# Kernel optimization log

Hardware: AMD Instinct MI355X
Metric: run time of the kernel (lower is better)

The kernel has to match this reference:

```python
import jax, jax.numpy as jnp
import numpy as np

B, S, D, H = 4, 2048, 1024, 16
HD = D // H  # head_dim = 64


def setup_inputs() -> dict:
    key = jax.random.key(0)
    kx, kq, kk, kv, ko = jax.random.split(key, 5)
    scale = 1.0 / np.sqrt(D)
    return {
        "x": jax.random.normal(kx, (B, S, D), dtype=jnp.float32),
        "wq": jax.random.normal(kq, (D, D), dtype=jnp.float32) * scale,
        "wk": jax.random.normal(kk, (D, D), dtype=jnp.float32) * scale,
        "wv": jax.random.normal(kv, (D, D), dtype=jnp.float32) * scale,
        "wo": jax.random.normal(ko, (D, D), dtype=jnp.float32) * scale,
    }


def reference(x, wq, wk, wv, wo):
    b, s, d = x.shape
    # nn.Linear stores weight [out, in]: y = x @ W.T
    q = (x @ wq.T).reshape(b, s, H, HD)
    k = (x @ wk.T).reshape(b, s, H, HD)
    v = (x @ wv.T).reshape(b, s, H, HD)
    # scores: [b, h, s, s]
    scores = jnp.einsum("bqhd,bkhd->bhqk", q, k) / np.sqrt(HD)
    causal = jnp.triu(jnp.ones((s, s), dtype=bool), k=1)
    scores = jnp.where(causal, -jnp.inf, scores)
    attn = jax.nn.softmax(scores, axis=-1)
    out = jnp.einsum("bhqk,bkhd->bqhd", attn, v).reshape(b, s, d)
    return out @ wo.T
```

## Files before the change

### kernel.cpp

```cpp
#include <hip/hip_runtime.h>
#include <math.h>

typedef unsigned short u16;
typedef __attribute__((ext_vector_type(8))) short short8;
typedef __attribute__((ext_vector_type(4))) short short4v;
typedef __attribute__((ext_vector_type(4))) float f32x4;
typedef __attribute__((ext_vector_type(2))) unsigned int uint2v;

constexpr int Bn = 4, Sn = 2048, Dn = 1024, Hn = 16;
constexpr float SCL = 0.125f * 1.44269504f;

__device__ __forceinline__ u16 f2bf(float f) {
  unsigned u = __float_as_uint(f);
  u += 0x7fffu + ((u >> 16) & 1u);
  return (u16)(u >> 16);
}

__device__ __forceinline__ f32x4 mfma32(short8 a, short8 b, f32x4 c) {
  return __builtin_amdgcn_mfma_f32_16x16x32_bf16(a, b, c, 0, 0, 0);
}

__device__ __forceinline__ f32x4 mfma16(short4v a, short4v b, f32x4 c) {
#if __has_builtin(__builtin_amdgcn_mfma_f32_16x16x16_bf16)
  return __builtin_amdgcn_mfma_f32_16x16x16_bf16(a, b, c, 0, 0, 0);
#elif __has_builtin(__builtin_amdgcn_mfma_f32_16x16x16bf16_1k)
  return __builtin_amdgcn_mfma_f32_16x16x16bf16_1k(a, b, c, 0, 0, 0);
#else
  short8 a8 = {a[0], a[1], a[2], a[3], 0, 0, 0, 0};
  short8 b8 = {b[0], b[1], b[2], b[3], 0, 0, 0, 0};
  return __builtin_amdgcn_mfma_f32_16x16x32_bf16(a8, b8, c, 0, 0, 0);
#endif
}

__device__ __forceinline__ void gl_lds16(const u16* g, u16* l) {
  __builtin_amdgcn_global_load_lds(
      (const __attribute__((address_space(1))) unsigned int*)g,
      (__attribute__((address_space(3))) unsigned int*)l, 16, 0, 0);
}

__global__ __launch_bounds__(256) void cast_all(
    const float4* __restrict__ x, const float4* __restrict__ wq,
    const float4* __restrict__ wk, const float4* __restrict__ wv,
    const float4* __restrict__ wo, ushort4* __restrict__ xb,
    ushort4* __restrict__ wqb, ushort4* __restrict__ wkb,
    ushort4* __restrict__ wvb, ushort4* __restrict__ wob) {
  const int blk = blockIdx.x;
  const float4* in;
  ushort4* out;
  int base;
  float s = 1.0f;
  if (blk < 8192) {
    in = x; out = xb; base = blk;
  } else if (blk < 9216) {
    in = wq; out = wqb; base = blk - 8192; s = SCL;
  } else if (blk < 10240) {
    in = wk; out = wkb; base = blk - 9216;
  } else if (blk < 11264) {
    in = wv; out = wvb; base = blk - 10240;
  } else {
    in = wo; out = wob; base = blk - 11264;
  }
  const int i = base * 256 + threadIdx.x;
  const float4 f = in[i];
  ushort4 o;
  o.x = f2bf(f.x * s); o.y = f2bf(f.y * s);
  o.z = f2bf(f.z * s); o.w = f2bf(f.w * s);
  out[i] = o;
}

template <int MODE>
__device__ __forceinline__ void gemm_body(const u16* __restrict__ A,
                                          const u16* __restrict__ W,
                                          u16* __restrict__ Cb,
                                          float* __restrict__ Cf,
                                          int bx, int by) {
  __shared__ u16 Asm[128 * 32];
  __shared__ u16 Wsm[128 * 32];
  const int t = threadIdx.x;
  const int w = t >> 6, l = t & 63;
  const int wy = w >> 1, wx = w & 1;
  const int q = l >> 4, r = l & 15;
  const int m0 = bx * 128, n0 = by * 128;
  const int c0 = w * 64 + l;

  f32x4 acc[4][4] = {};

  for (int k0 = 0; k0 < 1024; k0 += 32) {
    __syncthreads();
#pragma unroll
    for (int i = 0; i < 2; ++i) {
      const int c = c0 + i * 256;
      const int row = c >> 2, cl = c & 3;
      const int cg = cl ^ ((row >> 1) & 3);
      gl_lds16(A + (size_t)(m0 + row) * 1024 + k0 + cg * 8, &Asm[c * 8]);
      gl_lds16(W + (size_t)(n0 + row) * 1024 + k0 + cg * 8, &Wsm[c * 8]);
    }
    __syncthreads();

    short8 af[4], bf[4];
#pragma unroll
    for (int mi = 0; mi < 4; ++mi) {
      const int rowA = wy * 64 + mi * 16 + r;
      af[mi] = *(const short8*)&Asm[rowA * 32 + (q ^ ((rowA >> 1) & 3)) * 8];
      const int rowB = wx * 64 + mi * 16 + r;
      bf[mi] = *(const short8*)&Wsm[rowB * 32 + (q ^ ((rowB >> 1) & 3)) * 8];
    }
#pragma unroll
    for (int mi = 0; mi < 4; ++mi)
#pragma unroll
      for (int ni = 0; ni < 4; ++ni)
        acc[mi][ni] = mfma32(af[mi], bf[ni], acc[mi][ni]);
  }

  if (MODE == 2) {
    const int bq = m0 >> 11;
    const int jt = ((m0 & 2047) >> 6) + wy;
    const int hh = (n0 >> 6) + wx;
    u16* vt_t = Cb + ((size_t)((bq * 16 + hh) * 32) + jt) * 4096;
#pragma unroll
    for (int mi = 0; mi < 4; ++mi)
#pragma unroll
      for (int ni = 0; ni < 4; ++ni) {
        short4v pk;
#pragma unroll
        for (int e = 0; e < 4; ++e) pk[e] = (short)f2bf(acc[mi][ni][e]);
        const int hd = ni * 16 + r;
        const int c2 = q + 4 * (mi >> 1);
        *(short4v*)&vt_t[hd * 64 + ((c2 ^ (r & 7)) * 8) + (mi & 1) * 4] = pk;
      }
    return;
  }

#pragma unroll
  for (int mi = 0; mi < 4; ++mi) {
    const int row = m0 + wy * 64 + mi * 16 + q * 4;
#pragma unroll
    for (int ni = 0; ni < 4; ++ni) {
      const int col = n0 + wx * 64 + ni * 16 + r;
#pragma unroll
      for (int e = 0; e < 4; ++e) {
        if (MODE == 1)
          Cf[(size_t)(row + e) * 1024 + col] = acc[mi][ni][e];
        else
          Cb[(size_t)(row + e) * 1024 + col] = f2bf(acc[mi][ni][e]);
      }
    }
  }
}

__global__ __launch_bounds__(256) void gemm_qkv(const u16* __restrict__ A,
                                                const u16* __restrict__ Wq,
                                                const u16* __restrict__ Wk,
                                                const u16* __restrict__ Wv,
                                                u16* __restrict__ Cq,
                                                u16* __restrict__ Ck,
                                                u16* __restrict__ Vt) {
  const int z = blockIdx.z;
  if (z == 2)
    gemm_body<2>(A, Wv, Vt, nullptr, blockIdx.x, blockIdx.y);
  else
    gemm_body<0>(A, z ? Wk : Wq, z ? Ck : Cq, nullptr, blockIdx.x, blockIdx.y);
}

__global__ __launch_bounds__(256) void gemm_out(const u16* __restrict__ A,
                                                const u16* __restrict__ W,
                                                float* __restrict__ C) {
  gemm_body<1>(A, W, nullptr, C, blockIdx.x, blockIdx.y);
}

__global__ __launch_bounds__(128) void attn_v6(const u16* __restrict__ Qb,
                                               const u16* __restrict__ Kb,
                                               const u16* __restrict__ Vt,
                                               u16* __restrict__ Ob) {
  const int i = blockIdx.x;
  const int grp = (i & 7) + 8 * (i >> 7);
  const int qp = (i >> 3) & 15;
  const int b = grp >> 4, h = grp & 15;
  const int t = threadIdx.x;
  const int w = t >> 6, l = t & 63;
  const int q = l >> 4, r = l & 15;

  __shared__ u16 Kd[2][4096];
  __shared__ u16 Vd[2][4096];

  const size_t kgbase = (size_t)(b * Sn) * Dn + h * 64;
  const size_t vgbase = (size_t)((b * Hn + h) * 32) * 4096;

  const u16* kg[4];
  const u16* vg[4];
#pragma unroll
  for (int ii = 0; ii < 4; ++ii) {
    const int c = t + ii * 128, row = c >> 3, cl = c & 7;
    kg[ii] = Kb + kgbase + (size_t)row * Dn + (cl ^ (row & 7)) * 8;
    vg[ii] = Vt + vgbase + c * 8;
  }
  const int rx = r & 7;
  const int b0 = r * 64 + ((q ^ rx) * 8);
  const int b1 = r * 64 + (((4 + q) ^ rx) * 8);

#pragma unroll 1
  for (int ph = 0; ph < 2; ++ph) {
    const int st = ph ? 31 - qp : qp;
    const int qb64 = st * 64;

    short8 Qf[2][2];
#pragma unroll
    for (int mi = 0; mi < 2; ++mi)
#pragma unroll
      for (int kf = 0; kf < 2; ++kf)
        Qf[mi][kf] = *(const short8*)(Qb +
            (size_t)(b * Sn + qb64 + w * 32 + mi * 16 + r) * Dn + h * 64 +
            kf * 32 + q * 8);

    f32x4 O[2][4] = {};
    float l_[2] = {0.f, 0.f};

    __syncthreads();
#pragma unroll
    for (int ii = 0; ii < 4; ++ii) {
      const int c8 = (t + ii * 128) * 8;
      gl_lds16(kg[ii], &Kd[0][c8]);
      gl_lds16(vg[ii], &Vd[0][c8]);
    }
    const u16* kgt[4];
    const u16* vgt[4];
#pragma unroll
    for (int ii = 0; ii < 4; ++ii) {
      kgt[ii] = kg[ii] + 64 * Dn;
      vgt[ii] = vg[ii] + 4096;
    }

    for (int jt = 0; jt <= st; ++jt) {
      __syncthreads();
      if (jt < st) {
        u16* kl = &Kd[(jt + 1) & 1][0];
        u16* vl = &Vd[(jt + 1) & 1][0];
#pragma unroll
        for (int ii = 0; ii < 4; ++ii) {
          const int c8 = (t + ii * 128) * 8;
          gl_lds16(kgt[ii], kl + c8);
          gl_lds16(vgt[ii], vl + c8);
          kgt[ii] += 64 * Dn;
          vgt[ii] += 4096;
        }
      }
      const u16* KtA = &Kd[jt & 1][b0];
      const u16* KtB = &Kd[jt & 1][b1];

      short8 Kf[4][2];
#pragma unroll
      for (int ni = 0; ni < 4; ++ni) {
        Kf[ni][0] = *(const short8*)(KtA + ni * 1024);
        Kf[ni][1] = *(const short8*)(KtB + ni * 1024);
      }

      f32x4 S[2][4] = {};
      __builtin_amdgcn_s_setprio(1);
#pragma unroll
      for (int ni = 0; ni < 4; ++ni)
#pragma unroll
        for (int kf = 0; kf < 2; ++kf) {
          S[0][ni] = mfma32(Kf[ni][kf], Qf[0][kf], S[0][ni]);
          S[1][ni] = mfma32(Kf[ni][kf], Qf[1][kf], S[1][ni]);
        }
      __builtin_amdgcn_s_setprio(0);

      if (jt == st) {
#pragma unroll
        for (int mi = 0; mi < 2; ++mi) {
          const int qrow = w * 32 + mi * 16 + r;
#pragma unroll
          for (int ni = 0; ni < 4; ++ni) {
            const int key = ni * 16 + q * 4;
#pragma unroll
            for (int e = 0; e < 4; ++e)
              if (key + e > qrow) S[mi][ni][e] = -3.0e38f;
          }
        }
      }

      short4v Pf[2][4];
#pragma unroll
      for (int mi = 0; mi < 2; ++mi)
#pragma unroll
        for (int ni = 0; ni < 4; ++ni) {
          const float p0 = __builtin_amdgcn_exp2f(S[mi][ni][0]);
          const float p1 = __builtin_amdgcn_exp2f(S[mi][ni][1]);
          const float p2 = __builtin_amdgcn_exp2f(S[mi][ni][2]);
          const float p3 = __builtin_amdgcn_exp2f(S[mi][ni][3]);
          l_[mi] += (p0 + p1) + (p2 + p3);
          unsigned plo, phi;
          asm("v_cvt_pk_bf16_f32 %0, %1, %2" : "=v"(plo) : "v"(p0), "v"(p1));
          asm("v_cvt_pk_bf16_f32 %0, %1, %2" : "=v"(phi) : "v"(p2), "v"(p3));
          const uint2v pk2 = {plo, phi};
          Pf[mi][ni] = __builtin_bit_cast(short4v, pk2);
        }

      const u16* VsA = &Vd[jt & 1][b0];
      const u16* VsB = &Vd[jt & 1][b1];
      __builtin_amdgcn_s_setprio(1);
#pragma unroll
      for (int np = 0; np < 2; ++np)
#pragma unroll
        for (int ni2 = 0; ni2 < 4; ++ni2) {
          const short8 vv =
              *(const short8*)((np ? VsB : VsA) + ni2 * 1024);
          const short4v va = {vv[0], vv[1], vv[2], vv[3]};
          const short4v vb2 = {vv[4], vv[5], vv[6], vv[7]};
          O[0][ni2] = mfma16(va, Pf[0][2 * np], O[0][ni2]);
          O[0][ni2] = mfma16(vb2, Pf[0][2 * np + 1], O[0][ni2]);
          O[1][ni2] = mfma16(va, Pf[1][2 * np], O[1][ni2]);
          O[1][ni2] = mfma16(vb2, Pf[1][2 * np + 1], O[1][ni2]);
        }
      __builtin_amdgcn_s_setprio(0);
    }

#pragma unroll
    for (int mi = 0; mi < 2; ++mi) {
      float s = l_[mi];
      s += __shfl_xor(s, 16, 64);
      s += __shfl_xor(s, 32, 64);
      const float rl = __builtin_amdgcn_rcpf(s);
#pragma unroll
      for (int ni2 = 0; ni2 < 4; ++ni2) {
        short4v o;
#pragma unroll
        for (int e = 0; e < 4; ++e) o[e] = (short)f2bf(O[mi][ni2][e] * rl);
        *(short4v*)(Ob + (size_t)(b * Sn + qb64 + w * 32 + mi * 16 + r) * Dn +
                    h * 64 + ni2 * 16 + q * 4) = o;
      }
    }
  }
}

extern "C" void kernel_launch(void* const* d_in, const int* in_sizes, int n_in,
                              void* d_out, int out_size, void* d_ws, size_t ws_size,
                              hipStream_t stream) {
  const float* x  = (const float*)d_in[0];
  const float* wq = (const float*)d_in[1];
  const float* wk = (const float*)d_in[2];
  const float* wv = (const float*)d_in[3];
  const float* wo = (const float*)d_in[4];
  float* out = (float*)d_out;

  u16* xb  = (u16*)d_ws;
  u16* wqb = xb + 8388608;
  u16* wkb = wqb + 1048576;
  u16* wvb = wkb + 1048576;
  u16* wob = wvb + 1048576;
  u16* qb  = wob + 1048576;
  u16* kb  = qb + 8388608;
  u16* vt2 = kb + 8388608;
  u16* aob = vt2 + 8388608;

  cast_all<<<12288, 256, 0, stream>>>(
      (const float4*)x, (const float4*)wq, (const float4*)wk,
      (const float4*)wv, (const float4*)wo, (ushort4*)xb, (ushort4*)wqb,
      (ushort4*)wkb, (ushort4*)wvb, (ushort4*)wob);

  gemm_qkv<<<dim3(64, 8, 3), 256, 0, stream>>>(xb, wqb, wkb, wvb, qb, kb, vt2);

  attn_v6<<<1024, 128, 0, stream>>>(qb, kb, vt2, aob);

  gemm_out<<<dim3(64, 8), 256, 0, stream>>>(aob, wob, out);
}
```

Baseline: 240.8 us.

## Load attention K/V straight into registers, split query tiles into more blocks, widen GEMM K-step

The attention kernel drops LDS staging and barriers. Each wave now loads K and V fragments directly from global memory into registers, with K prefetched one tile ahead through a ping-pong register pair. Each block handles one query tile instead of two paired tiles, so the grid doubles, and an interleaved mapping keeps the load balanced. The V-transpose store drops its XOR swizzle to match the new direct-read pattern, and the QKV/out GEMMs move to a 64-wide K step with an 8-way swizzle, halving barrier count. Risks include redundant global K/V traffic across the two waves and higher register pressure.

```diff
diff --git a/kernel.cpp b/kernel.cpp
--- a/kernel.cpp
+++ b/kernel.cpp
@@ -74,42 +74,43 @@
                                           u16* __restrict__ Cb,
                                           float* __restrict__ Cf,
                                           int bx, int by) {
-  __shared__ u16 Asm[128 * 32];
-  __shared__ u16 Wsm[128 * 32];
+  __shared__ u16 Asm[128 * 64];
+  __shared__ u16 Wsm[128 * 64];
   const int t = threadIdx.x;
   const int w = t >> 6, l = t & 63;
   const int wy = w >> 1, wx = w & 1;
   const int q = l >> 4, r = l & 15;
   const int m0 = bx * 128, n0 = by * 128;
-  const int c0 = w * 64 + l;
 
   f32x4 acc[4][4] = {};
 
-  for (int k0 = 0; k0 < 1024; k0 += 32) {
+  for (int k0 = 0; k0 < 1024; k0 += 64) {
     __syncthreads();
 #pragma unroll
-    for (int i = 0; i < 2; ++i) {
-      const int c = c0 + i * 256;
-      const int row = c >> 2, cl = c & 3;
-      const int cg = cl ^ ((row >> 1) & 3);
+    for (int i = 0; i < 4; ++i) {
+      const int c = t + i * 256;
+      const int row = c >> 3, cl = c & 7;
+      const int cg = cl ^ (row & 7);
       gl_lds16(A + (size_t)(m0 + row) * 1024 + k0 + cg * 8, &Asm[c * 8]);
       gl_lds16(W + (size_t)(n0 + row) * 1024 + k0 + cg * 8, &Wsm[c * 8]);
     }
     __syncthreads();
-
-    short8 af[4], bf[4];
-#pragma unroll
-    for (int mi = 0; mi < 4; ++mi) {
-      const int rowA = wy * 64 + mi * 16 + r;
-      af[mi] = *(const short8*)&Asm[rowA * 32 + (q ^ ((rowA >> 1) & 3)) * 8];
-      const int rowB = wx * 64 + mi * 16 + r;
-      bf[mi] = *(const short8*)&Wsm[rowB * 32 + (q ^ ((rowB >> 1) & 3)) * 8];
-    }
-#pragma unroll
-    for (int mi = 0; mi < 4; ++mi)
-#pragma unroll
-      for (int ni = 0; ni < 4; ++ni)
-        acc[mi][ni] = mfma32(af[mi], bf[ni], acc[mi][ni]);
+#pragma unroll
+    for (int kf = 0; kf < 2; ++kf) {
+      short8 af[4], bf[4];
+#pragma unroll
+      for (int mi = 0; mi < 4; ++mi) {
+        const int rowA = wy * 64 + mi * 16 + r;
+        af[mi] = *(const short8*)&Asm[rowA * 64 + ((kf * 4 + q) ^ (rowA & 7)) * 8];
+        const int rowB = wx * 64 + mi * 16 + r;
+        bf[mi] = *(const short8*)&Wsm[rowB * 64 + ((kf * 4 + q) ^ (rowB & 7)) * 8];
+      }
+#pragma unroll
+      for (int mi = 0; mi < 4; ++mi)
+#pragma unroll
+        for (int ni = 0; ni < 4; ++ni)
+          acc[mi][ni] = mfma32(af[mi], bf[ni], acc[mi][ni]);
+    }
   }
 
   if (MODE == 2) {
@@ -126,7 +127,7 @@
         for (int e = 0; e < 4; ++e) pk[e] = (short)f2bf(acc[mi][ni][e]);
         const int hd = ni * 16 + r;
         const int c2 = q + 4 * (mi >> 1);
-        *(short4v*)&vt_t[hd * 64 + ((c2 ^ (r & 7)) * 8) + (mi & 1) * 4] = pk;
+        *(short4v*)&vt_t[hd * 64 + c2 * 8 + (mi & 1) * 4] = pk;
       }
     return;
   }
@@ -168,167 +169,141 @@
   gemm_body<1>(A, W, nullptr, C, blockIdx.x, blockIdx.y);
 }
 
-__global__ __launch_bounds__(128) void attn_v6(const u16* __restrict__ Qb,
-                                               const u16* __restrict__ Kb,
-                                               const u16* __restrict__ Vt,
-                                               u16* __restrict__ Ob) {
+__global__ __launch_bounds__(128, 3) void attn_v7(const u16* __restrict__ Qb,
+                                                  const u16* __restrict__ Kb,
+                                                  const u16* __restrict__ Vt,
+                                                  u16* __restrict__ Ob) {
   const int i = blockIdx.x;
-  const int grp = (i & 7) + 8 * (i >> 7);
-  const int qp = (i >> 3) & 15;
-  const int b = grp >> 4, h = grp & 15;
+  const int xcd = i & 7;
+  const int j = i >> 3;
+  const int g = 8 * (j >> 5) + xcd;
+  const int k = j & 31;
+  const int st = (k & 1) ? 31 - (k >> 1) : (k >> 1);
+  const int b = g >> 4, h = g & 15;
   const int t = threadIdx.x;
   const int w = t >> 6, l = t & 63;
   const int q = l >> 4, r = l & 15;
 
-  __shared__ u16 Kd[2][4096];
-  __shared__ u16 Vd[2][4096];
-
-  const size_t kgbase = (size_t)(b * Sn) * Dn + h * 64;
-  const size_t vgbase = (size_t)((b * Hn + h) * 32) * 4096;
-
-  const u16* kg[4];
-  const u16* vg[4];
-#pragma unroll
-  for (int ii = 0; ii < 4; ++ii) {
-    const int c = t + ii * 128, row = c >> 3, cl = c & 7;
-    kg[ii] = Kb + kgbase + (size_t)row * Dn + (cl ^ (row & 7)) * 8;
-    vg[ii] = Vt + vgbase + c * 8;
-  }
-  const int rx = r & 7;
-  const int b0 = r * 64 + ((q ^ rx) * 8);
-  const int b1 = r * 64 + (((4 + q) ^ rx) * 8);
-
-#pragma unroll 1
-  for (int ph = 0; ph < 2; ++ph) {
-    const int st = ph ? 31 - qp : qp;
-    const int qb64 = st * 64;
-
-    short8 Qf[2][2];
+  const int qb64 = st * 64;
+
+  short8 Qf[2][2];
+#pragma unroll
+  for (int mi = 0; mi < 2; ++mi)
+#pragma unroll
+    for (int kf = 0; kf < 2; ++kf)
+      Qf[mi][kf] = *(const short8*)(Qb +
+          (size_t)(b * Sn + qb64 + w * 32 + mi * 16 + r) * Dn + h * 64 +
+          kf * 32 + q * 8);
+
+  f32x4 O[2][4] = {};
+  float l_[2] = {0.f, 0.f};
+
+  const u16* Kg = Kb + (size_t)(b * Sn) * Dn + h * 64 + (size_t)r * Dn + q * 8;
+  const u16* Vg = Vt + (size_t)((b * Hn + h) * 32) * 4096 + r * 64 + q * 8;
+
+  short8 Ka[4][2], Kn[4][2];
+#pragma unroll
+  for (int ni = 0; ni < 4; ++ni)
+#pragma unroll
+    for (int kf = 0; kf < 2; ++kf)
+      Ka[ni][kf] = *(const short8*)(Kg + ni * 16384 + kf * 32);
+
+  auto tile = [&](short8(&Kc)[4][2], short8(&Kp)[4][2], const int jt) {
+    short8 vv[2][4];
+    const u16* vt = Vg + (size_t)jt * 4096;
+#pragma unroll
+    for (int np = 0; np < 2; ++np)
+#pragma unroll
+      for (int ni2 = 0; ni2 < 4; ++ni2)
+        vv[np][ni2] = *(const short8*)(vt + ni2 * 1024 + np * 32);
+
+    f32x4 S[2][4] = {};
+    __builtin_amdgcn_s_setprio(1);
+#pragma unroll
+    for (int ni = 0; ni < 4; ++ni)
+#pragma unroll
+      for (int kf = 0; kf < 2; ++kf) {
+        S[0][ni] = mfma32(Kc[ni][kf], Qf[0][kf], S[0][ni]);
+        S[1][ni] = mfma32(Kc[ni][kf], Qf[1][kf], S[1][ni]);
+      }
+    __builtin_amdgcn_s_setprio(0);
+
+    if (jt < st) {
+      const u16* kt = Kg + (size_t)(jt + 1) * 65536;
+#pragma unroll
+      for (int ni = 0; ni < 4; ++ni)
+#pragma unroll
+        for (int kf = 0; kf < 2; ++kf)
+          Kp[ni][kf] = *(const short8*)(kt + ni * 16384 + kf * 32);
+    }
+
+    if (jt == st) {
+#pragma unroll
+      for (int mi = 0; mi < 2; ++mi) {
+        const int qrow = w * 32 + mi * 16 + r;
+#pragma unroll
+        for (int ni = 0; ni < 4; ++ni) {
+          const int key = ni * 16 + q * 4;
+#pragma unroll
+          for (int e = 0; e < 4; ++e)
+            if (key + e > qrow) S[mi][ni][e] = -3.0e38f;
+        }
+      }
+    }
+
+    short4v Pf[2][4];
 #pragma unroll
     for (int mi = 0; mi < 2; ++mi)
 #pragma unroll
-      for (int kf = 0; kf < 2; ++kf)
-        Qf[mi][kf] = *(const short8*)(Qb +
-            (size_t)(b * Sn + qb64 + w * 32 + mi * 16 + r) * Dn + h * 64 +
-            kf * 32 + q * 8);
-
-    f32x4 O[2][4] = {};
-    float l_[2] = {0.f, 0.f};
-
-    __syncthreads();
-#pragma unroll
-    for (int ii = 0; ii < 4; ++ii) {
-      const int c8 = (t + ii * 128) * 8;
-      gl_lds16(kg[ii], &Kd[0][c8]);
-      gl_lds16(vg[ii], &Vd[0][c8]);
-    }
-    const u16* kgt[4];
-    const u16* vgt[4];
-#pragma unroll
-    for (int ii = 0; ii < 4; ++ii) {
-      kgt[ii] = kg[ii] + 64 * Dn;
-      vgt[ii] = vg[ii] + 4096;
-    }
-
-    for (int jt = 0; jt <= st; ++jt) {
-      __syncthreads();
-      if (jt < st) {
-        u16* kl = &Kd[(jt + 1) & 1][0];
-        u16* vl = &Vd[(jt + 1) & 1][0];
-#pragma unroll
-        for (int ii = 0; ii < 4; ++ii) {
-          const int c8 = (t + ii * 128) * 8;
-          gl_lds16(kgt[ii], kl + c8);
-          gl_lds16(vgt[ii], vl + c8);
-          kgt[ii] += 64 * Dn;
-          vgt[ii] += 4096;
-        }
-      }
-      const u16* KtA = &Kd[jt & 1][b0];
-      const u16* KtB = &Kd[jt & 1][b1];
-
-      short8 Kf[4][2];
-#pragma unroll
       for (int ni = 0; ni < 4; ++ni) {
-        Kf[ni][0] = *(const short8*)(KtA + ni * 1024);
-        Kf[ni][1] = *(const short8*)(KtB + ni * 1024);
-      }
-
-      f32x4 S[2][4] = {};
-      __builtin_amdgcn_s_setprio(1);
-#pragma unroll
-      for (int ni = 0; ni < 4; ++ni)
-#pragma unroll
-        for (int kf = 0; kf < 2; ++kf) {
-          S[0][ni] = mfma32(Kf[ni][kf], Qf[0][kf], S[0][ni]);
-          S[1][ni] = mfma32(Kf[ni][kf], Qf[1][kf], S[1][ni]);
-        }
-      __builtin_amdgcn_s_setprio(0);
-
-      if (jt == st) {
-#pragma unroll
-        for (int mi = 0; mi < 2; ++mi) {
-          const int qrow = w * 32 + mi * 16 + r;
-#pragma unroll
-          for (int ni = 0; ni < 4; ++ni) {
-            const int key = ni * 16 + q * 4;
-#pragma unroll
-            for (int e = 0; e < 4; ++e)
-              if (key + e > qrow) S[mi][ni][e] = -3.0e38f;
-          }
-        }
-      }
-
-      short4v Pf[2][4];
-#pragma unroll
-      for (int mi = 0; mi < 2; ++mi)
-#pragma unroll
-        for (int ni = 0; ni < 4; ++ni) {
-          const float p0 = __builtin_amdgcn_exp2f(S[mi][ni][0]);
-          const float p1 = __builtin_amdgcn_exp2f(S[mi][ni][1]);
-          const float p2 = __builtin_amdgcn_exp2f(S[mi][ni][2]);
-          const float p3 = __builtin_amdgcn_exp2f(S[mi][ni][3]);
-          l_[mi] += (p0 + p1) + (p2 + p3);
-          unsigned plo, phi;
-          asm("v_cvt_pk_bf16_f32 %0, %1, %2" : "=v"(plo) : "v"(p0), "v"(p1));
-          asm("v_cvt_pk_bf16_f32 %0, %1, %2" : "=v"(phi) : "v"(p2), "v"(p3));
-          const uint2v pk2 = {plo, phi};
-          Pf[mi][ni] = __builtin_bit_cast(short4v, pk2);
-        }
-
-      const u16* VsA = &Vd[jt & 1][b0];
-      const u16* VsB = &Vd[jt & 1][b1];
-      __builtin_amdgcn_s_setprio(1);
-#pragma unroll
-      for (int np = 0; np < 2; ++np)
-#pragma unroll
-        for (int ni2 = 0; ni2 < 4; ++ni2) {
-          const short8 vv =
-              *(const short8*)((np ? VsB : VsA) + ni2 * 1024);
-          const short4v va = {vv[0], vv[1], vv[2], vv[3]};
-          const short4v vb2 = {vv[4], vv[5], vv[6], vv[7]};
-          O[0][ni2] = mfma16(va, Pf[0][2 * np], O[0][ni2]);
-          O[0][ni2] = mfma16(vb2, Pf[0][2 * np + 1], O[0][ni2]);
-          O[1][ni2] = mfma16(va, Pf[1][2 * np], O[1][ni2]);
-          O[1][ni2] = mfma16(vb2, Pf[1][2 * np + 1], O[1][ni2]);
-        }
-      __builtin_amdgcn_s_setprio(0);
-    }
-
-#pragma unroll
-    for (int mi = 0; mi < 2; ++mi) {
-      float s = l_[mi];
-      s += __shfl_xor(s, 16, 64);
-      s += __shfl_xor(s, 32, 64);
-      const float rl = __builtin_amdgcn_rcpf(s);
+        const float p0 = __builtin_amdgcn_exp2f(S[mi][ni][0]);
+        const float p1 = __builtin_amdgcn_exp2f(S[mi][ni][1]);
+        const float p2 = __builtin_amdgcn_exp2f(S[mi][ni][2]);
+        const float p3 = __builtin_amdgcn_exp2f(S[mi][ni][3]);
+        l_[mi] += (p0 + p1) + (p2 + p3);
+        unsigned plo, phi;
+        asm("v_cvt_pk_bf16_f32 %0, %1, %2" : "=v"(plo) : "v"(p0), "v"(p1));
+        asm("v_cvt_pk_bf16_f32 %0, %1, %2" : "=v"(phi) : "v"(p2), "v"(p3));
+        const uint2v pk2 = {plo, phi};
+        Pf[mi][ni] = __builtin_bit_cast(short4v, pk2);
+      }
+
+    __builtin_amdgcn_s_setprio(1);
+#pragma unroll
+    for (int np = 0; np < 2; ++np)
 #pragma unroll
       for (int ni2 = 0; ni2 < 4; ++ni2) {
-        short4v o;
-#pragma unroll
-        for (int e = 0; e < 4; ++e) o[e] = (short)f2bf(O[mi][ni2][e] * rl);
-        *(short4v*)(Ob + (size_t)(b * Sn + qb64 + w * 32 + mi * 16 + r) * Dn +
-                    h * 64 + ni2 * 16 + q * 4) = o;
-      }
+        const short8 vvx = vv[np][ni2];
+        const short4v va = {vvx[0], vvx[1], vvx[2], vvx[3]};
+        const short4v vb2 = {vvx[4], vvx[5], vvx[6], vvx[7]};
+        O[0][ni2] = mfma16(va, Pf[0][2 * np], O[0][ni2]);
+        O[0][ni2] = mfma16(vb2, Pf[0][2 * np + 1], O[0][ni2]);
+        O[1][ni2] = mfma16(va, Pf[1][2 * np], O[1][ni2]);
+        O[1][ni2] = mfma16(vb2, Pf[1][2 * np + 1], O[1][ni2]);
+      }
+    __builtin_amdgcn_s_setprio(0);
+  };
+
+  int jt = 0;
+  for (; jt + 1 <= st; jt += 2) {
+    tile(Ka, Kn, jt);
+    tile(Kn, Ka, jt + 1);
+  }
+  if (jt <= st) tile(Ka, Kn, jt);
+
+#pragma unroll
+  for (int mi = 0; mi < 2; ++mi) {
+    float s = l_[mi];
+    s += __shfl_xor(s, 16, 64);
+    s += __shfl_xor(s, 32, 64);
+    const float rl = __builtin_amdgcn_rcpf(s);
+#pragma unroll
+    for (int ni2 = 0; ni2 < 4; ++ni2) {
+      short4v o;
+#pragma unroll
+      for (int e = 0; e < 4; ++e) o[e] = (short)f2bf(O[mi][ni2][e] * rl);
+      *(short4v*)(Ob + (size_t)(b * Sn + qb64 + w * 32 + mi * 16 + r) * Dn +
+                  h * 64 + ni2 * 16 + q * 4) = o;
     }
   }
 }
@@ -360,7 +335,7 @@
 
   gemm_qkv<<<dim3(64, 8, 3), 256, 0, stream>>>(xb, wqb, wkb, wvb, qb, kb, vt2);
 
-  attn_v6<<<1024, 128, 0, stream>>>(qb, kb, vt2, aob);
+  attn_v7<<<2048, 128, 0, stream>>>(qb, kb, vt2, aob);
 
   gemm_out<<<dim3(64, 8), 256, 0, stream>>>(aob, wob, out);
 }
```

Result: slower. 615.1 us (+155.4%).

## Double-buffer LDS tiles in projection GEMM to overlap loads with MFMA

Applied to the files above, without the earlier changes.

Splits the shared-memory A and W tiles into two buffers and issues the global-to-LDS loads for the next K slice before computing on the current one. This leaves one barrier per iteration instead of two and is meant to hide global load latency behind the MFMA work. It doubles LDS use per block, which may lower occupancy. It also depends on the barrier at the end of each iteration to make the direct-to-LDS loads visible, with no explicit vmcnt wait.

```diff
diff --git a/kernel.cpp b/kernel.cpp
--- a/kernel.cpp
+++ b/kernel.cpp
@@ -74,42 +74,60 @@
                                           u16* __restrict__ Cb,
                                           float* __restrict__ Cf,
                                           int bx, int by) {
-  __shared__ u16 Asm[128 * 32];
-  __shared__ u16 Wsm[128 * 32];
+  __shared__ u16 Asm[2][128 * 32];
+  __shared__ u16 Wsm[2][128 * 32];
   const int t = threadIdx.x;
   const int w = t >> 6, l = t & 63;
   const int wy = w >> 1, wx = w & 1;
   const int q = l >> 4, r = l & 15;
   const int m0 = bx * 128, n0 = by * 128;
-  const int c0 = w * 64 + l;
 
   f32x4 acc[4][4] = {};
 
-  for (int k0 = 0; k0 < 1024; k0 += 32) {
-    __syncthreads();
-#pragma unroll
-    for (int i = 0; i < 2; ++i) {
-      const int c = c0 + i * 256;
-      const int row = c >> 2, cl = c & 3;
-      const int cg = cl ^ ((row >> 1) & 3);
-      gl_lds16(A + (size_t)(m0 + row) * 1024 + k0 + cg * 8, &Asm[c * 8]);
-      gl_lds16(W + (size_t)(n0 + row) * 1024 + k0 + cg * 8, &Wsm[c * 8]);
-    }
-    __syncthreads();
-
+  const u16* asrc[2];
+  const u16* wsrc[2];
+  int dst[2];
+#pragma unroll
+  for (int i = 0; i < 2; ++i) {
+    const int c = t + i * 256;
+    const int row = c >> 2, cl = c & 3;
+    const int cg = cl ^ ((row >> 1) & 3);
+    asrc[i] = A + (size_t)(m0 + row) * 1024 + cg * 8;
+    wsrc[i] = W + (size_t)(n0 + row) * 1024 + cg * 8;
+    dst[i] = c * 8;
+  }
+
+#pragma unroll
+  for (int i = 0; i < 2; ++i) {
+    gl_lds16(asrc[i], &Asm[0][dst[i]]);
+    gl_lds16(wsrc[i], &Wsm[0][dst[i]]);
+  }
+  __syncthreads();
+
+  for (int it = 0; it < 32; ++it) {
+    const int cur = it & 1;
+    if (it < 31) {
+      const int k0 = (it + 1) * 32;
+#pragma unroll
+      for (int i = 0; i < 2; ++i) {
+        gl_lds16(asrc[i] + k0, &Asm[cur ^ 1][dst[i]]);
+        gl_lds16(wsrc[i] + k0, &Wsm[cur ^ 1][dst[i]]);
+      }
+    }
     short8 af[4], bf[4];
 #pragma unroll
     for (int mi = 0; mi < 4; ++mi) {
       const int rowA = wy * 64 + mi * 16 + r;
-      af[mi] = *(const short8*)&Asm[rowA * 32 + (q ^ ((rowA >> 1) & 3)) * 8];
+      af[mi] = *(const short8*)&Asm[cur][rowA * 32 + (q ^ ((rowA >> 1) & 3)) * 8];
       const int rowB = wx * 64 + mi * 16 + r;
-      bf[mi] = *(const short8*)&Wsm[rowB * 32 + (q ^ ((rowB >> 1) & 3)) * 8];
+      bf[mi] = *(const short8*)&Wsm[cur][rowB * 32 + (q ^ ((rowB >> 1) & 3)) * 8];
     }
 #pragma unroll
     for (int mi = 0; mi < 4; ++mi)
 #pragma unroll
       for (int ni = 0; ni < 4; ++ni)
         acc[mi][ni] = mfma32(af[mi], bf[ni], acc[mi][ni]);
+    __syncthreads();
   }
 
   if (MODE == 2) {
```

Result: slower. 268.2 us (+11.3%).

## Split attention into one query tile per block and deepen GEMM K-step

Applied to the files above, without the earlier changes.

The attention kernel no longer pairs a short and a long query tile inside one block. It launches 2048 blocks, each handling a single 64-row query tile, ordered longest-first so the hardware scheduler can balance the causal work, while keeping the XCD-aware grouping. The GEMM bodies move to a 64-wide K step with LDS tiles sized in the kernels, an 8-way XOR swizzle and two MFMA sub-steps per barrier pair. This halves the number of syncs per GEMM at the cost of twice the LDS per block, which may reduce occupancy.

```diff
diff --git a/kernel.cpp b/kernel.cpp
--- a/kernel.cpp
+++ b/kernel.cpp
@@ -73,43 +73,44 @@
                                           const u16* __restrict__ W,
                                           u16* __restrict__ Cb,
                                           float* __restrict__ Cf,
-                                          int bx, int by) {
-  __shared__ u16 Asm[128 * 32];
-  __shared__ u16 Wsm[128 * 32];
+                                          int bx, int by,
+                                          u16* __restrict__ Asm,
+                                          u16* __restrict__ Wsm) {
   const int t = threadIdx.x;
   const int w = t >> 6, l = t & 63;
   const int wy = w >> 1, wx = w & 1;
   const int q = l >> 4, r = l & 15;
   const int m0 = bx * 128, n0 = by * 128;
-  const int c0 = w * 64 + l;
 
   f32x4 acc[4][4] = {};
 
-  for (int k0 = 0; k0 < 1024; k0 += 32) {
+  for (int k0 = 0; k0 < 1024; k0 += 64) {
     __syncthreads();
 #pragma unroll
-    for (int i = 0; i < 2; ++i) {
-      const int c = c0 + i * 256;
-      const int row = c >> 2, cl = c & 3;
-      const int cg = cl ^ ((row >> 1) & 3);
+    for (int i = 0; i < 4; ++i) {
+      const int c = t + i * 256;
+      const int row = c >> 3, cl = c & 7;
+      const int cg = cl ^ (row & 7);
       gl_lds16(A + (size_t)(m0 + row) * 1024 + k0 + cg * 8, &Asm[c * 8]);
       gl_lds16(W + (size_t)(n0 + row) * 1024 + k0 + cg * 8, &Wsm[c * 8]);
     }
     __syncthreads();
-
-    short8 af[4], bf[4];
-#pragma unroll
-    for (int mi = 0; mi < 4; ++mi) {
-      const int rowA = wy * 64 + mi * 16 + r;
-      af[mi] = *(const short8*)&Asm[rowA * 32 + (q ^ ((rowA >> 1) & 3)) * 8];
-      const int rowB = wx * 64 + mi * 16 + r;
-      bf[mi] = *(const short8*)&Wsm[rowB * 32 + (q ^ ((rowB >> 1) & 3)) * 8];
-    }
-#pragma unroll
-    for (int mi = 0; mi < 4; ++mi)
-#pragma unroll
-      for (int ni = 0; ni < 4; ++ni)
-        acc[mi][ni] = mfma32(af[mi], bf[ni], acc[mi][ni]);
+#pragma unroll
+    for (int kf = 0; kf < 2; ++kf) {
+      short8 af[4], bf[4];
+#pragma unroll
+      for (int mi = 0; mi < 4; ++mi) {
+        const int rowA = wy * 64 + mi * 16 + r;
+        af[mi] = *(const short8*)&Asm[rowA * 64 + ((kf * 4 + q) ^ (rowA & 7)) * 8];
+        const int rowB = wx * 64 + mi * 16 + r;
+        bf[mi] = *(const short8*)&Wsm[rowB * 64 + ((kf * 4 + q) ^ (rowB & 7)) * 8];
+      }
+#pragma unroll
+      for (int mi = 0; mi < 4; ++mi)
+#pragma unroll
+        for (int ni = 0; ni < 4; ++ni)
+          acc[mi][ni] = mfma32(af[mi], bf[ni], acc[mi][ni]);
+    }
   }
 
   if (MODE == 2) {
@@ -155,26 +156,34 @@
                                                 u16* __restrict__ Cq,
                                                 u16* __restrict__ Ck,
                                                 u16* __restrict__ Vt) {
+  __shared__ u16 Asm[128 * 64];
+  __shared__ u16 Wsm[128 * 64];
   const int z = blockIdx.z;
   if (z == 2)
-    gemm_body<2>(A, Wv, Vt, nullptr, blockIdx.x, blockIdx.y);
+    gemm_body<2>(A, Wv, Vt, nullptr, blockIdx.x, blockIdx.y, Asm, Wsm);
   else
-    gemm_body<0>(A, z ? Wk : Wq, z ? Ck : Cq, nullptr, blockIdx.x, blockIdx.y);
+    gemm_body<0>(A, z ? Wk : Wq, z ? Ck : Cq, nullptr, blockIdx.x, blockIdx.y,
+                 Asm, Wsm);
 }
 
 __global__ __launch_bounds__(256) void gemm_out(const u16* __restrict__ A,
                                                 const u16* __restrict__ W,
                                                 float* __restrict__ C) {
-  gemm_body<1>(A, W, nullptr, C, blockIdx.x, blockIdx.y);
-}
-
-__global__ __launch_bounds__(128) void attn_v6(const u16* __restrict__ Qb,
+  __shared__ u16 Asm[128 * 64];
+  __shared__ u16 Wsm[128 * 64];
+  gemm_body<1>(A, W, nullptr, C, blockIdx.x, blockIdx.y, Asm, Wsm);
+}
+
+__global__ __launch_bounds__(128) void attn_v8(const u16* __restrict__ Qb,
                                                const u16* __restrict__ Kb,
                                                const u16* __restrict__ Vt,
                                                u16* __restrict__ Ob) {
   const int i = blockIdx.x;
-  const int grp = (i & 7) + 8 * (i >> 7);
-  const int qp = (i >> 3) & 15;
+  const int xcd = i & 7;
+  const int k = (i >> 3) & 31;
+  const int gl = i >> 8;
+  const int grp = xcd + 8 * gl;
+  const int st = 31 - k;
   const int b = grp >> 4, h = grp & 15;
   const int t = threadIdx.x;
   const int w = t >> 6, l = t & 63;
@@ -198,137 +207,132 @@
   const int b0 = r * 64 + ((q ^ rx) * 8);
   const int b1 = r * 64 + (((4 + q) ^ rx) * 8);
 
-#pragma unroll 1
-  for (int ph = 0; ph < 2; ++ph) {
-    const int st = ph ? 31 - qp : qp;
-    const int qb64 = st * 64;
-
-    short8 Qf[2][2];
+  const int qb64 = st * 64;
+
+  short8 Qf[2][2];
+#pragma unroll
+  for (int mi = 0; mi < 2; ++mi)
+#pragma unroll
+    for (int kf = 0; kf < 2; ++kf)
+      Qf[mi][kf] = *(const short8*)(Qb +
+          (size_t)(b * Sn + qb64 + w * 32 + mi * 16 + r) * Dn + h * 64 +
+          kf * 32 + q * 8);
+
+  f32x4 O[2][4] = {};
+  float l_[2] = {0.f, 0.f};
+
+#pragma unroll
+  for (int ii = 0; ii < 4; ++ii) {
+    const int c8 = (t + ii * 128) * 8;
+    gl_lds16(kg[ii], &Kd[0][c8]);
+    gl_lds16(vg[ii], &Vd[0][c8]);
+  }
+  const u16* kgt[4];
+  const u16* vgt[4];
+#pragma unroll
+  for (int ii = 0; ii < 4; ++ii) {
+    kgt[ii] = kg[ii] + 64 * Dn;
+    vgt[ii] = vg[ii] + 4096;
+  }
+
+  for (int jt = 0; jt <= st; ++jt) {
+    __syncthreads();
+    if (jt < st) {
+      u16* kl = &Kd[(jt + 1) & 1][0];
+      u16* vl = &Vd[(jt + 1) & 1][0];
+#pragma unroll
+      for (int ii = 0; ii < 4; ++ii) {
+        const int c8 = (t + ii * 128) * 8;
+        gl_lds16(kgt[ii], kl + c8);
+        gl_lds16(vgt[ii], vl + c8);
+        kgt[ii] += 64 * Dn;
+        vgt[ii] += 4096;
+      }
+    }
+    const u16* KtA = &Kd[jt & 1][b0];
+    const u16* KtB = &Kd[jt & 1][b1];
+
+    short8 Kf[4][2];
+#pragma unroll
+    for (int ni = 0; ni < 4; ++ni) {
+      Kf[ni][0] = *(const short8*)(KtA + ni * 1024);
+      Kf[ni][1] = *(const short8*)(KtB + ni * 1024);
+    }
+
+    f32x4 S[2][4] = {};
+    __builtin_amdgcn_s_setprio(1);
+#pragma unroll
+    for (int ni = 0; ni < 4; ++ni)
+#pragma unroll
+      for (int kf = 0; kf < 2; ++kf) {
+        S[0][ni] = mfma32(Kf[ni][kf], Qf[0][kf], S[0][ni]);
+        S[1][ni] = mfma32(Kf[ni][kf], Qf[1][kf], S[1][ni]);
+      }
+    __builtin_amdgcn_s_setprio(0);
+
+    if (jt == st) {
+#pragma unroll
+      for (int mi = 0; mi < 2; ++mi) {
+        const int qrow = w * 32 + mi * 16 + r;
+#pragma unroll
+        for (int ni = 0; ni < 4; ++ni) {
+          const int key = ni * 16 + q * 4;
+#pragma unroll
+          for (int e = 0; e < 4; ++e)
+            if (key + e > qrow) S[mi][ni][e] = -3.0e38f;
+        }
+      }
+    }
+
+    short4v Pf[2][4];
 #pragma unroll
     for (int mi = 0; mi < 2; ++mi)
 #pragma unroll
-      for (int kf = 0; kf < 2; ++kf)
-        Qf[mi][kf] = *(const short8*)(Qb +
-            (size_t)(b * Sn + qb64 + w * 32 + mi * 16 + r) * Dn + h * 64 +
-            kf * 32 + q * 8);
-
-    f32x4 O[2][4] = {};
-    float l_[2] = {0.f, 0.f};
-
-    __syncthreads();
-#pragma unroll
-    for (int ii = 0; ii < 4; ++ii) {
-      const int c8 = (t + ii * 128) * 8;
-      gl_lds16(kg[ii], &Kd[0][c8]);
-      gl_lds16(vg[ii], &Vd[0][c8]);
-    }
-    const u16* kgt[4];
-    const u16* vgt[4];
-#pragma unroll
-    for (int ii = 0; ii < 4; ++ii) {
-      kgt[ii] = kg[ii] + 64 * Dn;
-      vgt[ii] = vg[ii] + 4096;
-    }
-
-    for (int jt = 0; jt <= st; ++jt) {
-      __syncthreads();
-      if (jt < st) {
-        u16* kl = &Kd[(jt + 1) & 1][0];
-        u16* vl = &Vd[(jt + 1) & 1][0];
-#pragma unroll
-        for (int ii = 0; ii < 4; ++ii) {
-          const int c8 = (t + ii * 128) * 8;
-          gl_lds16(kgt[ii], kl + c8);
-          gl_lds16(vgt[ii], vl + c8);
-          kgt[ii] += 64 * Dn;
-          vgt[ii] += 4096;
-        }
-      }
-      const u16* KtA = &Kd[jt & 1][b0];
-      const u16* KtB = &Kd[jt & 1][b1];
-
-      short8 Kf[4][2];
-#pragma unroll
       for (int ni = 0; ni < 4; ++ni) {
-        Kf[ni][0] = *(const short8*)(KtA + ni * 1024);
-        Kf[ni][1] = *(const short8*)(KtB + ni * 1024);
-      }
-
-      f32x4 S[2][4] = {};
-      __builtin_amdgcn_s_setprio(1);
-#pragma unroll
-      for (int ni = 0; ni < 4; ++ni)
-#pragma unroll
-        for (int kf = 0; kf < 2; ++kf) {
-          S[0][ni] = mfma32(Kf[ni][kf], Qf[0][kf], S[0][ni]);
-          S[1][ni] = mfma32(Kf[ni][kf], Qf[1][kf], S[1][ni]);
-        }
-      __builtin_amdgcn_s_setprio(0);
-
-      if (jt == st) {
-#pragma unroll
-        for (int mi = 0; mi < 2; ++mi) {
-          const int qrow = w * 32 + mi * 16 + r;
-#pragma unroll
-          for (int ni = 0; ni < 4; ++ni) {
-            const int key = ni * 16 + q * 4;
-#pragma unroll
-            for (int e = 0; e < 4; ++e)
-              if (key + e > qrow) S[mi][ni][e] = -3.0e38f;
-          }
-        }
-      }
-
-      short4v Pf[2][4];
-#pragma unroll
-      for (int mi = 0; mi < 2; ++mi)
-#pragma unroll
-        for (int ni = 0; ni < 4; ++ni) {
-          const float p0 = __builtin_amdgcn_exp2f(S[mi][ni][0]);
-          const float p1 = __builtin_amdgcn_exp2f(S[mi][ni][1]);
-          const float p2 = __builtin_amdgcn_exp2f(S[mi][ni][2]);
-          const float p3 = __builtin_amdgcn_exp2f(S[mi][ni][3]);
-          l_[mi] += (p0 + p1) + (p2 + p3);
-          unsigned plo, phi;
-          asm("v_cvt_pk_bf16_f32 %0, %1, %2" : "=v"(plo) : "v"(p0), "v"(p1));
-          asm("v_cvt_pk_bf16_f32 %0, %1, %2" : "=v"(phi) : "v"(p2), "v"(p3));
-          const uint2v pk2 = {plo, phi};
-          Pf[mi][ni] = __builtin_bit_cast(short4v, pk2);
-        }
-
-      const u16* VsA = &Vd[jt & 1][b0];
-      const u16* VsB = &Vd[jt & 1][b1];
-      __builtin_amdgcn_s_setprio(1);
-#pragma unroll
-      for (int np = 0; np < 2; ++np)
-#pragma unroll
-        for (int ni2 = 0; ni2 < 4; ++ni2) {
-          const short8 vv =
-              *(const short8*)((np ? VsB : VsA) + ni2 * 1024);
-          const short4v va = {vv[0], vv[1], vv[2], vv[3]};
-          const short4v vb2 = {vv[4], vv[5], vv[6], vv[7]};
-          O[0][ni2] = mfma16(va, Pf[0][2 * np], O[0][ni2]);
-          O[0][ni2] = mfma16(vb2, Pf[0][2 * np + 1], O[0][ni2]);
-          O[1][ni2] = mfma16(va, Pf[1][2 * np], O[1][ni2]);
-          O[1][ni2] = mfma16(vb2, Pf[1][2 * np + 1], O[1][ni2]);
-        }
-      __builtin_amdgcn_s_setprio(0);
-    }
-
-#pragma unroll
-    for (int mi = 0; mi < 2; ++mi) {
-      float s = l_[mi];
-      s += __shfl_xor(s, 16, 64);
-      s += __shfl_xor(s, 32, 64);
-      const float rl = __builtin_amdgcn_rcpf(s);
+        const float p0 = __builtin_amdgcn_exp2f(S[mi][ni][0]);
+        const float p1 = __builtin_amdgcn_exp2f(S[mi][ni][1]);
+        const float p2 = __builtin_amdgcn_exp2f(S[mi][ni][2]);
+        const float p3 = __builtin_amdgcn_exp2f(S[mi][ni][3]);
+        l_[mi] += (p0 + p1) + (p2 + p3);
+        unsigned plo, phi;
+        asm("v_cvt_pk_bf16_f32 %0, %1, %2" : "=v"(plo) : "v"(p0), "v"(p1));
+        asm("v_cvt_pk_bf16_f32 %0, %1, %2" : "=v"(phi) : "v"(p2), "v"(p3));
+        const uint2v pk2 = {plo, phi};
+        Pf[mi][ni] = __builtin_bit_cast(short4v, pk2);
+      }
+
+    const u16* VsA = &Vd[jt & 1][b0];
+    const u16* VsB = &Vd[jt & 1][b1];
+    __builtin_amdgcn_s_setprio(1);
+#pragma unroll
+    for (int np = 0; np < 2; ++np)
 #pragma unroll
       for (int ni2 = 0; ni2 < 4; ++ni2) {
-        short4v o;
-#pragma unroll
-        for (int e = 0; e < 4; ++e) o[e] = (short)f2bf(O[mi][ni2][e] * rl);
-        *(short4v*)(Ob + (size_t)(b * Sn + qb64 + w * 32 + mi * 16 + r) * Dn +
-                    h * 64 + ni2 * 16 + q * 4) = o;
-      }
+        const short8 vv =
+            *(const short8*)((np ? VsB : VsA) + ni2 * 1024);
+        const short4v va = {vv[0], vv[1], vv[2], vv[3]};
+        const short4v vb2 = {vv[4], vv[5], vv[6], vv[7]};
+        O[0][ni2] = mfma16(va, Pf[0][2 * np], O[0][ni2]);
+        O[0][ni2] = mfma16(vb2, Pf[0][2 * np + 1], O[0][ni2]);
+        O[1][ni2] = mfma16(va, Pf[1][2 * np], O[1][ni2]);
+        O[1][ni2] = mfma16(vb2, Pf[1][2 * np + 1], O[1][ni2]);
+      }
+    __builtin_amdgcn_s_setprio(0);
+  }
+
+#pragma unroll
+  for (int mi = 0; mi < 2; ++mi) {
+    float s = l_[mi];
+    s += __shfl_xor(s, 16, 64);
+    s += __shfl_xor(s, 32, 64);
+    const float rl = __builtin_amdgcn_rcpf(s);
+#pragma unroll
+    for (int ni2 = 0; ni2 < 4; ++ni2) {
+      short4v o;
+#pragma unroll
+      for (int e = 0; e < 4; ++e) o[e] = (short)f2bf(O[mi][ni2][e] * rl);
+      *(short4v*)(Ob + (size_t)(b * Sn + qb64 + w * 32 + mi * 16 + r) * Dn +
+                  h * 64 + ni2 * 16 + q * 4) = o;
     }
   }
 }
@@ -360,7 +364,7 @@
 
   gemm_qkv<<<dim3(64, 8, 3), 256, 0, stream>>>(xb, wqb, wkb, wvb, qb, kb, vt2);
 
-  attn_v6<<<1024, 128, 0, stream>>>(qb, kb, vt2, aob);
+  attn_v8<<<2048, 128, 0, stream>>>(qb, kb, vt2, aob);
 
   gemm_out<<<dim3(64, 8), 256, 0, stream>>>(aob, wob, out);
 }
```

Measured after the change: 270.7 us. 12.4% more time.
